# Performance work log

Measured on AMD Instinct MI355X. Metric: run time of the kernel, lower is better.

The kernel has to match this reference:

```python
import jax, jax.numpy as jnp
import numpy as np

N, M, A, F = 8000, 12, 64, 64
EPS = 1e-5


def setup_inputs() -> dict:
    key = jax.random.key(0)
    ks = jax.random.split(key, 8)
    rn = lambda k, s, sc=0.05: jax.random.normal(k, s, jnp.float32) * sc
    return {
        "atom_in_fea": rn(ks[0], (N, A), 1.0),
        "nbr_fea": rn(ks[1], (N, M, F), 1.0),
        "nbr_fea_idx": jax.random.randint(ks[2], (N, M), 0, N),
        # fc_full: in = 2A+F, out = 2A (stored as (in, out))
        "W_full": rn(ks[3], (2 * A + F, 2 * A)), "b_full": jnp.zeros((2 * A,), jnp.float32),
        "bn1_gamma": jnp.ones((2 * A,), jnp.float32), "bn1_beta": jnp.zeros((2 * A,), jnp.float32),
        # fc_edge: in = 2A+F, out = 2F
        "W_edge": rn(ks[4], (2 * A + F, 2 * F)), "b_edge": jnp.zeros((2 * F,), jnp.float32),
        "bne_gamma": jnp.ones((2 * F,), jnp.float32), "bne_beta": jnp.zeros((2 * F,), jnp.float32),
        # fc_3body: in = 3A+2F, out = 2A
        "W_3body": rn(ks[5], (3 * A + 2 * F, 2 * A)), "b_3body": jnp.zeros((2 * A,), jnp.float32),
        "bn3_gamma": jnp.ones((2 * A,), jnp.float32), "bn3_beta": jnp.zeros((2 * A,), jnp.float32),
        # bn2 over atom_fea_len
        "bn2_gamma": jnp.ones((A,), jnp.float32), "bn2_beta": jnp.zeros((A,), jnp.float32),
    }


def _bn(x, gamma, beta):
    # training-mode BatchNorm1d: batch stats over all but the last (channel) axis, biased var
    axes = tuple(range(x.ndim - 1))
    mean = jnp.mean(x, axes, keepdims=True)
    var = jnp.mean(jnp.square(x - mean), axes, keepdims=True)
    return (x - mean) * jax.lax.rsqrt(var + EPS) * gamma + beta


def _gate(z, axis):
    filt, core = jnp.split(z, 2, axis=-1)
    return jnp.sum(jax.nn.sigmoid(filt) * jax.nn.softplus(core), axis=axis)


def reference(atom_in_fea, nbr_fea, nbr_fea_idx,
              W_full, b_full, bn1_gamma, bn1_beta,
              W_edge, b_edge, bne_gamma, bne_beta,
              W_3body, b_3body, bn3_gamma, bn3_beta,
              bn2_gamma, bn2_beta):
    a_len = atom_in_fea.shape[1]
    f_len = nbr_fea.shape[2]
    atom_nbr = atom_in_fea[nbr_fea_idx]                       # (N, M, A) gather
    total = jnp.concatenate([
        jnp.broadcast_to(atom_in_fea[:, None, :], atom_nbr.shape),
        atom_nbr, nbr_fea], axis=-1)                           # (N, M, 2A+F)

    # 2-body gated update
    g = _bn(total @ W_full + b_full, bn1_gamma, bn1_beta)      # (N, M, 2A)
    two_body = _gate(g, axis=1)                                # (N, A)

    # explicit edge update
    e = _bn(total @ W_edge + b_edge, bne_gamma, bne_beta)      # (N, M, 2F)
    ef, ec = jnp.split(e, 2, axis=-1)
    nbr_out_fea = nbr_fea + jax.nn.sigmoid(ef) * jax.nn.softplus(ec)

    # 3-body term: Linear over concat([x_i, x_j, x_l, e_ij, e_il]) decomposed so we never
    # materialize the (N, M, M, 3A+2F) concat; only the (N, M, M, 2A) projection exists.
    Wa, Wj, Wl, Wij, Wil = jnp.split(
        W_3body, [a_len, 2 * a_len, 3 * a_len, 3 * a_len + f_len], axis=0)
    p_i = atom_in_fea @ Wa                                     # (N, 2A)
    p_j = atom_nbr @ Wj + nbr_fea @ Wij                        # (N, M, 2A) j/ij part
    p_l = atom_nbr @ Wl + nbr_fea @ Wil                        # (N, M, 2A) l/il part
    z = p_i[:, None, None, :] + p_j[:, :, None, :] + p_l[:, None, :, :] + b_3body
    z = _bn(z, bn3_gamma, bn3_beta)                            # (N, M, M, 2A)
    three_body = _gate(z, axis=(1, 2))                         # (N, A)

    total_summed = _bn(two_body + three_body, bn2_gamma, bn2_beta)
    atom_out_fea = jax.nn.softplus(atom_in_fea + total_summed)
    return (atom_out_fea, nbr_out_fea)
```

## Files before the change

kernel.cpp:

```cpp
#include <hip/hip_runtime.h>

typedef unsigned short u16;
typedef unsigned int u32;
typedef __attribute__((ext_vector_type(8))) short short8;
typedef __attribute__((ext_vector_type(4))) float f32x4;

#define NATOMS 8000
#define MNBR 12
#define EPSV 1e-5f
#define AB 4
#define ROWS 48
#define NBLK 2000
#define K2REC 1664

#define GRP_B 1056
#define STG_B 12672
__device__ __forceinline__ int stg_idx(int row, int col) {
  return (row >> 2) * 528 + (row & 3) * 128 + col;
}

#define PA_OFF 0
#define WTA_OFF 12288000
#define WTE_OFF 12386304
#define SSUM_OFF 12451840
#define PARAMS_OFF 12459008
#define TBUF_OFF 12462080
#define WS_NEED 14510080

#define SS_BN1S 0
#define SS_BN1S2 128
#define SS_BNES 256
#define SS_BNES2 384
#define SS_U2 512
#define SS_V2 640
#define SS_A 768
#define SS_A2 896
#define SS_UB 1024
#define SS_VB 1152
#define SS_AU 1280
#define SS_AV 1408
#define SS_UV 1536

__device__ __forceinline__ u16 f2bf(float f) {
  u32 u = __float_as_uint(f);
  u += 0x7FFFu + ((u >> 16) & 1u);
  return (u16)(u >> 16);
}
__device__ __forceinline__ float bf2f(u16 h) { return __uint_as_float(((u32)h) << 16); }

__device__ __forceinline__ float sigf(float x) {
  return __builtin_amdgcn_rcpf(1.f + __expf(-x));
}
__device__ __forceinline__ float spf(float x) {
  return fmaxf(x, 0.f) + __logf(1.f + __expf(-fabsf(x)));
}

__device__ __forceinline__ void mfma16(f32x4 &acc, short8 a, short8 b) {
  asm volatile("v_mfma_f32_16x16x32_bf16 %0, %1, %2, %0" : "+v"(acc) : "v"(a), "v"(b));
}
__device__ __forceinline__ void accfence(f32x4 &a) {
  asm volatile("s_nop 7\ns_nop 7\ns_nop 7" : "+v"(a));
}
__device__ __forceinline__ void initfence(f32x4 &a) {
  asm volatile("s_nop 1" : "+v"(a));
}

typedef __attribute__((address_space(3))) unsigned int lds_uint;
typedef __attribute__((address_space(1))) const unsigned int glob_uint;
__device__ __forceinline__ void dma16(const void* g, void* l) {
  __builtin_amdgcn_global_load_lds((glob_uint*)g, (lds_uint*)l, 16, 0, 0);
}

__device__ __forceinline__ void load_idx3(const int* __restrict__ nidx, int eb, int w, int l,
                                          int (&ai)[3]) {
#pragma unroll
  for (int i = 0; i < 3; ++i) ai[i] = nidx[eb + (w * 3 + i) * 4 + (l >> 4)];
}
__device__ __forceinline__ void dma_slice(const u16* __restrict__ PA, const int (&ai)[3],
                                          char* st, int off, int w, int l) {
#pragma unroll
  for (int i = 0; i < 3; ++i) {
    const u16* base = PA + (size_t)ai[i] * 768 + ((l & 15) << 3);
    dma16(base + off, (u16*)st + (w * 3 + i) * 528);
  }
}
__device__ __forceinline__ void dma_own2(const u16* __restrict__ PA, u16* paown0, u16* paown1,
                                         int ab, int l) {
  const u16* src = PA + (size_t)(ab + (l >> 4)) * 768 + ((l & 15) << 3);
  dma16(src, paown0);
  dma16(src + 256, paown1);
}
__device__ __forceinline__ void wait_A_barrier() {
  asm volatile("s_waitcnt vmcnt(3)" ::: "memory");
  __builtin_amdgcn_s_barrier();
}

__device__ __forceinline__ void stage_row16(short* lds, int row, int c16, const float* __restrict__ src) {
  const float4* s4 = reinterpret_cast<const float4*>(src);
  float4 q0 = s4[0], q1 = s4[1], q2 = s4[2], q3 = s4[3];
  short8 lo, hi;
  lo[0]=(short)f2bf(q0.x); lo[1]=(short)f2bf(q0.y); lo[2]=(short)f2bf(q0.z); lo[3]=(short)f2bf(q0.w);
  lo[4]=(short)f2bf(q1.x); lo[5]=(short)f2bf(q1.y); lo[6]=(short)f2bf(q1.z); lo[7]=(short)f2bf(q1.w);
  hi[0]=(short)f2bf(q2.x); hi[1]=(short)f2bf(q2.y); hi[2]=(short)f2bf(q2.z); hi[3]=(short)f2bf(q2.w);
  hi[4]=(short)f2bf(q3.x); hi[5]=(short)f2bf(q3.y); hi[6]=(short)f2bf(q3.z); hi[7]=(short)f2bf(q3.w);
  int base = row * 128 + c16 * 2;
  int sw = (row & 7) << 4;
  *reinterpret_cast<short8*>(reinterpret_cast<char*>(lds) + (base ^ sw)) = lo;
  *reinterpret_cast<short8*>(reinterpret_cast<char*>(lds) + ((base + 16) ^ sw)) = hi;
}

__device__ __forceinline__ short8 lds_afrag(const short* lds, int row, int kbyte) {
  int off = (row * 128 + kbyte) ^ ((row & 7) << 4);
  return *reinterpret_cast<const short8*>(reinterpret_cast<const char*>(lds) + off);
}

template <int RT>
__device__ __forceinline__ void mfma_block(const short* nbrT, const u16* __restrict__ WTE,
                                           int b, int w, int l, f32x4 (&acc)[RT][2]) {
  short8 bfr[2][2];
#pragma unroll
  for (int p = 0; p < 2; ++p) {
    int wr = b * 128 + ((w + p * 4) << 4) + (l & 15);
#pragma unroll
    for (int kc = 0; kc < 2; ++kc)
      bfr[p][kc] = *reinterpret_cast<const short8*>(WTE + (size_t)wr * 64 + kc * 32 + ((l >> 4) << 3));
  }
#pragma unroll
  for (int rt = 0; rt < RT; ++rt)
#pragma unroll
    for (int p = 0; p < 2; ++p) { acc[rt][p] = f32x4{0.f, 0.f, 0.f, 0.f}; initfence(acc[rt][p]); }
#pragma unroll
  for (int rt = 0; rt < RT; ++rt) {
    int arow = rt * 16 + (l & 15);
    short8 a0 = lds_afrag(nbrT, arow, (l >> 4) << 4);
    short8 a1 = lds_afrag(nbrT, arow, 64 + ((l >> 4) << 4));
#pragma unroll
    for (int p = 0; p < 2; ++p) {
      mfma16(acc[rt][p], a0, bfr[p][0]);
      mfma16(acc[rt][p], a1, bfr[p][1]);
    }
  }
#pragma unroll
  for (int rt = 0; rt < RT; ++rt)
#pragma unroll
    for (int p = 0; p < 2; ++p) accfence(acc[rt][p]);
}

__global__ __launch_bounds__(256) void k0_prep(const float* __restrict__ W_full,
                                               const float* __restrict__ W_edge,
                                               const float* __restrict__ W_3body,
                                               u16* __restrict__ WTA, u16* __restrict__ WTE,
                                               float* __restrict__ ssum) {
  int t = blockIdx.x * 256 + threadIdx.x;
  if (t < 1792) ssum[t] = 0.f;
  if (t < 49152) {
    int col = t >> 6, k = t & 63;
    int blk = col >> 7, c = col & 127;
    float v;
    switch (blk) {
      case 0: v = W_full[k * 128 + c]; break;
      case 1: v = W_full[(64 + k) * 128 + c]; break;
      case 2: v = W_edge[k * 128 + c]; break;
      case 3: v = W_edge[(64 + k) * 128 + c]; break;
      case 4: v = W_3body[(64 + k) * 128 + c]; break;
      default: v = W_3body[(128 + k) * 128 + c]; break;
    }
    WTA[t] = f2bf(v);
  } else if (t < 49152 + 32768) {
    int u = t - 49152;
    int col = u >> 6, k = u & 63;
    int blk = col >> 7, c = col & 127;
    float v;
    switch (blk) {
      case 0: v = W_full[(128 + k) * 128 + c]; break;
      case 1: v = W_edge[(128 + k) * 128 + c]; break;
      case 2: v = W_3body[(192 + k) * 128 + c]; break;
      default: v = W_3body[(256 + k) * 128 + c]; break;
    }
    WTE[u] = f2bf(v);
  }
}

__global__ __launch_bounds__(256) void k1_pa(const float* __restrict__ atom_in,
                                             const u16* __restrict__ WTA,
                                             u16* __restrict__ PA) {
  __shared__ __align__(16) short xt[16 * 64];
  int t = threadIdx.x, l = t & 63, w = t >> 6;
  int ab = blockIdx.x * 16;
  if (t < 64) {
    int row = t >> 2, c16 = (t & 3) * 16;
    stage_row16(xt, row, c16, atom_in + (size_t)(ab + row) * 64 + c16);
  }
  __syncthreads();
  short8 a0 = lds_afrag(xt, l & 15, (l >> 4) << 4);
  short8 a1 = lds_afrag(xt, l & 15, 64 + ((l >> 4) << 4));
  for (int q = 0; q < 12; ++q) {
    int colg = (w * 12 + q) * 16 + (l & 15);
    short8 b0 = *reinterpret_cast<const short8*>(WTA + (size_t)colg * 64 + ((l >> 4) << 3));
    short8 b1 = *reinterpret_cast<const short8*>(WTA + (size_t)colg * 64 + 32 + ((l >> 4) << 3));
    f32x4 acc = f32x4{0.f, 0.f, 0.f, 0.f};
    initfence(acc);
    mfma16(acc, a0, b0);
    mfma16(acc, a1, b1);
    accfence(acc);
#pragma unroll
    for (int r = 0; r < 4; ++r) {
      int row = ((l >> 4) << 2) + r;
      PA[(size_t)(ab + row) * 768 + colg] = f2bf(acc[r]);
    }
  }
}

__global__ __launch_bounds__(256, 4) void k2a_stats(const float* __restrict__ nbr_fea,
                                                    const int* __restrict__ nidx,
                                                    const float* __restrict__ b_full,
                                                    const float* __restrict__ b_edge,
                                                    const u16* __restrict__ PA,
                                                    const u16* __restrict__ WTE,
                                                    float* __restrict__ k2scr) {
  __shared__ __align__(16) char smem[33536];
  short* nbrT = (short*)smem;
  u16* paown0 = (u16*)(smem + 31488);
  u16* paown1 = (u16*)(smem + 32512);
  int t = threadIdx.x, l = t & 63, w = t >> 6;
  int ab = blockIdx.x * AB, eb = ab * 12;
  float* sc = k2scr + (size_t)blockIdx.x * K2REC;

  for (int u = t; u < ROWS * 4; u += 256) {
    int row = u >> 2, c16 = (u & 3) * 16;
    stage_row16(nbrT, row, c16, nbr_fea + (size_t)(eb + row) * 64 + c16);
  }
  int ai[3];
  load_idx3(nidx, eb, w, l, ai);
  dma_slice(PA, ai, smem + 6144, 128, w, l);
  if (w == 0) dma_own2(PA, paown0, paown1, ab, l);
  dma_slice(PA, ai, smem + 18816, 384, w, l);
  wait_A_barrier();

#pragma unroll
  for (int b = 0; b < 2; ++b) {
    const u16* stg = (const u16*)(smem + 6144 + b * STG_B);
    const u16* po = b ? paown1 : paown0;
    f32x4 acc[3][2];
    mfma_block<3>(nbrT, WTE, b, w, l, acc);
    int col0 = (w << 4) + (l & 15), col1 = col0 + 64;
    int g = l >> 4;
    const float* bp = b ? b_edge : b_full;
    float bias0 = bp[col0], bias1 = bp[col1];
    float vs0 = 0.f, vs1 = 0.f, q0 = 0.f, q1 = 0.f;
#pragma unroll
    for (int rt = 0; rt < 3; ++rt) {
      int a12 = (rt * 16 + g * 4) / 12;
      float o0 = bf2f(po[a12 * 128 + col0]) + bias0;
      float o1 = bf2f(po[a12 * 128 + col1]) + bias1;
#pragma unroll
      for (int r = 0; r < 4; ++r) {
        int row = rt * 16 + g * 4 + r;
        float v0 = acc[rt][0][r] + bf2f(stg[stg_idx(row, col0)]) + o0;
        float v1 = acc[rt][1][r] + bf2f(stg[stg_idx(row, col1)]) + o1;
        vs0 += v0; q0 += v0 * v0; vs1 += v1; q1 += v1 * v1;
      }
    }
    vs0 += __shfl_xor(vs0, 16); vs0 += __shfl_xor(vs0, 32);
    vs1 += __shfl_xor(vs1, 16); vs1 += __shfl_xor(vs1, 32);
    q0 += __shfl_xor(q0, 16); q0 += __shfl_xor(q0, 32);
    q1 += __shfl_xor(q1, 16); q1 += __shfl_xor(q1, 32);
    if (l < 16) {
      int base = b ? 256 : 0;
      sc[base + col0] = vs0;
      sc[base + 128 + col0] = q0;
      sc[base + col1] = vs1;
      sc[base + 128 + col1] = q1;
    }
    if (b == 0) __syncthreads();
  }
}

__global__ __launch_bounds__(256, 4) void k2b_stats(const float* __restrict__ atom_in,
                                                    const float* __restrict__ nbr_fea,
                                                    const int* __restrict__ nidx,
                                                    const float* __restrict__ W_3body,
                                                    const float* __restrict__ b_3body,
                                                    const u16* __restrict__ PA,
                                                    const u16* __restrict__ WTE,
                                                    float* __restrict__ k2scr) {
  __shared__ __align__(16) char smem[36608];
  short* nbrT   = (short*)smem;
  float* ubar   = (float*)(smem + 31488);
  float* vbar   = (float*)(smem + 33536);
  float* xown   = (float*)(smem + 35584);
  float* redscr = (float*)(smem + 6144);
  int t = threadIdx.x, l = t & 63, w = t >> 6;
  int ab = blockIdx.x * AB, eb = ab * 12;
  float* sc = k2scr + (size_t)blockIdx.x * K2REC;

  for (int u = t; u < ROWS * 4; u += 256) {
    int row = u >> 2, c16 = (u & 3) * 16;
    stage_row16(nbrT, row, c16, nbr_fea + (size_t)(eb + row) * 64 + c16);
  }
  ubar[t] = 0.f; ubar[256 + t] = 0.f; vbar[t] = 0.f; vbar[256 + t] = 0.f;
  xown[t] = atom_in[(size_t)ab * 64 + t];
  int ai[3];
  load_idx3(nidx, eb, w, l, ai);
  dma_slice(PA, ai, smem + 6144, 512, w, l);
  dma_slice(PA, ai, smem + 18816, 640, w, l);
  wait_A_barrier();

#pragma unroll
  for (int b = 2; b < 4; ++b) {
    const u16* stg = (const u16*)(smem + 6144 + (b - 2) * STG_B);
    float* uvb = (b == 2) ? ubar : vbar;
    f32x4 acc[3][2];
    mfma_block<3>(nbrT, WTE, b, w, l, acc);
    int col0 = (w << 4) + (l & 15), col1 = col0 + 64;
    int g = l >> 4;
    float q0 = 0.f, q1 = 0.f;
#pragma unroll
    for (int rt = 0; rt < 3; ++rt) {
      int a12 = (rt * 16 + g * 4) / 12;
      float s0 = 0.f, s1 = 0.f;
#pragma unroll
      for (int r = 0; r < 4; ++r) {
        int row = rt * 16 + g * 4 + r;
        float v0 = acc[rt][0][r] + bf2f(stg[stg_idx(row, col0)]);
        float v1 = acc[rt][1][r] + bf2f(stg[stg_idx(row, col1)]);
        s0 += v0; q0 += v0 * v0; s1 += v1; q1 += v1 * v1;
      }
      atomicAdd(&uvb[a12 * 128 + col0], s0);
      atomicAdd(&uvb[a12 * 128 + col1], s1);
    }
    q0 += __shfl_xor(q0, 16); q0 += __shfl_xor(q0, 32);
    q1 += __shfl_xor(q1, 16); q1 += __shfl_xor(q1, 32);
    if (l < 16) {
      int base = (b == 2) ? SS_U2 : SS_V2;
      sc[base + col0] = q0;
      sc[base + col1] = q1;
    }
    if (b == 2) __syncthreads();
  }
  __syncthreads();

  {
    int c = t & 127, h = t >> 7;
    float dv0 = 0.f, dv1 = 0.f;
#pragma unroll 4
    for (int k = 0; k < 64; ++k) {
      float wk = W_3body[k * 128 + c];
      dv0 += xown[(2 * h) * 64 + k] * wk;
      dv1 += xown[(2 * h + 1) * 64 + k] * wk;
    }
    float b3v = b_3body[c];
    float pA = 0.f, pA2 = 0.f, pUb = 0.f, pVb = 0.f, pAU = 0.f, pAV = 0.f, pUV = 0.f;
#pragma unroll
    for (int aa = 0; aa < 2; ++aa) {
      int a = 2 * h + aa;
      float aval = (aa ? dv1 : dv0) + b3v;
      float ub = ubar[a * 128 + c] * (1.f / 12.f);
      float vb = vbar[a * 128 + c] * (1.f / 12.f);
      pA += aval; pA2 += aval * aval; pUb += ub; pVb += vb;
      pAU += aval * ub; pAV += aval * vb; pUV += ub * vb;
    }
    if (h == 1) {
      float* rs = &redscr[c * 7];
      rs[0] = pA; rs[1] = pA2; rs[2] = pUb; rs[3] = pVb; rs[4] = pAU; rs[5] = pAV; rs[6] = pUV;
    }
    __syncthreads();
    if (h == 0) {
      const float* rs = &redscr[c * 7];
      sc[SS_A + c] = pA + rs[0];
      sc[SS_A2 + c] = pA2 + rs[1];
      sc[SS_UB + c] = pUb + rs[2];
      sc[SS_VB + c] = pVb + rs[3];
      sc[SS_AU + c] = pAU + rs[4];
      sc[SS_AV + c] = pAV + rs[5];
      sc[SS_UV + c] = pUV + rs[6];
    }
  }
}

__global__ __launch_bounds__(256) void k3r_reduce(const float* __restrict__ k2scr,
                                                  float* __restrict__ ssum) {
  int cb = blockIdx.x & 1, ch = blockIdx.x >> 1;
  int f = cb * 256 + threadIdx.x;
  if (f >= K2REC / 4) return;
  int r0 = ch * 32;
  if (r0 >= NBLK) return;
  int r1 = min(r0 + 32, NBLK);
  float s0 = 0.f, s1 = 0.f, s2 = 0.f, s3 = 0.f;
#pragma unroll 8
  for (int r = r0; r < r1; ++r) {
    float4 v = *reinterpret_cast<const float4*>(k2scr + (size_t)r * K2REC + f * 4);
    s0 += v.x; s1 += v.y; s2 += v.z; s3 += v.w;
  }
  atomicAdd(&ssum[f * 4 + 0], s0);
  atomicAdd(&ssum[f * 4 + 1], s1);
  atomicAdd(&ssum[f * 4 + 2], s2);
  atomicAdd(&ssum[f * 4 + 3], s3);
}

__global__ void k3p_params(const float* __restrict__ ssum,
                           const float* __restrict__ g1, const float* __restrict__ be1,
                           const float* __restrict__ ge, const float* __restrict__ bee,
                           const float* __restrict__ g3, const float* __restrict__ be3,
                           float* __restrict__ params) {
  int c = threadIdx.x;
  if (c >= 128) return;
  const float cnt1 = 1.f / 96000.f;
  {
    float m = ssum[SS_BN1S + c] * cnt1;
    float var = ssum[SS_BN1S2 + c] * cnt1 - m * m;
    float s = g1[c] * rsqrtf(fmaxf(var, 0.f) + EPSV);
    params[c] = s; params[128 + c] = be1[c] - m * s;
  }
  {
    float m = ssum[SS_BNES + c] * cnt1;
    float var = ssum[SS_BNES2 + c] * cnt1 - m * m;
    float s = ge[c] * rsqrtf(fmaxf(var, 0.f) + EPSV);
    params[256 + c] = s; params[384 + c] = bee[c] - m * s;
  }
  {
    float Nf = (float)NATOMS;
    float A_ = ssum[SS_A + c], A2 = ssum[SS_A2 + c];
    float U2 = ssum[SS_U2 + c], V2 = ssum[SS_V2 + c];
    float Ub = ssum[SS_UB + c], Vb = ssum[SS_VB + c];
    float AU = ssum[SS_AU + c], AV = ssum[SS_AV + c], UV = ssum[SS_UV + c];
    float m = (A_ + Ub + Vb) / Nf;
    float ez2 = A2 / Nf + (U2 + V2) / (Nf * 12.f) + 2.f * (AU + AV + UV) / Nf;
    float var = ez2 - m * m;
    float s = g3[c] * rsqrtf(fmaxf(var, 0.f) + EPSV);
    params[512 + c] = s; params[640 + c] = be3[c] - m * s;
  }
}

__global__ __launch_bounds__(256, 4) void k4a_main(const float* __restrict__ nbr_fea,
                                                   const int* __restrict__ nidx,
                                                   const float* __restrict__ b_full,
                                                   const float* __restrict__ b_edge,
                                                   const u16* __restrict__ PA,
                                                   const u16* __restrict__ WTE,
                                                   const float* __restrict__ params,
                                                   float* __restrict__ tbuf,
                                                   float* __restrict__ out_nbr) {
  __shared__ __align__(16) char smem[36608];
  short* nbrT     = (short*)smem;
  u16* paown0     = (u16*)(smem + 31488);
  u16* paown1     = (u16*)(smem + 32512);
  float* t2buf    = (float*)(smem + 33536);
  float* params_s = (float*)(smem + 34560);
  int t = threadIdx.x, l = t & 63, w = t >> 6;
  int ab = blockIdx.x * AB, eb = ab * 12;

  for (int u = t; u < ROWS * 4; u += 256) {
    int row = u >> 2, c16 = (u & 3) * 16;
    stage_row16(nbrT, row, c16, nbr_fea + (size_t)(eb + row) * 64 + c16);
  }
  params_s[t] = params[t];
  params_s[t + 256] = params[t + 256];
  t2buf[t] = 0.f;
  int ai[3];
  load_idx3(nidx, eb, w, l, ai);
  dma_slice(PA, ai, smem + 6144, 128, w, l);
  if (w == 0) dma_own2(PA, paown0, paown1, ab, l);
  dma_slice(PA, ai, smem + 18816, 384, w, l);
  wait_A_barrier();

#pragma unroll
  for (int b = 0; b < 2; ++b) {
    const u16* stg = (const u16*)(smem + 6144 + b * STG_B);
    const u16* po = b ? paown1 : paown0;
    f32x4 acc[3][2];
    mfma_block<3>(nbrT, WTE, b, w, l, acc);
    int col0 = (w << 4) + (l & 15), col1 = col0 + 64;
    int g = l >> 4;
    const float* bp = b ? b_edge : b_full;
    float bias0 = bp[col0], bias1 = bp[col1];
    float sc0 = params_s[b * 256 + col0], sh0 = params_s[b * 256 + 128 + col0];
    float sc1 = params_s[b * 256 + col1], sh1 = params_s[b * 256 + 128 + col1];
#pragma unroll
    for (int rt = 0; rt < 3; ++rt) {
      int a12 = (rt * 16 + g * 4) / 12;
      float o0 = bf2f(po[a12 * 128 + col0]) + bias0;
      float o1 = bf2f(po[a12 * 128 + col1]) + bias1;
      float gsum = 0.f;
#pragma unroll
      for (int r = 0; r < 4; ++r) {
        int row = rt * 16 + g * 4 + r;
        float v0 = acc[rt][0][r] + bf2f(stg[stg_idx(row, col0)]) + o0;
        float v1 = acc[rt][1][r] + bf2f(stg[stg_idx(row, col1)]) + o1;
        float gate = sigf(v0 * sc0 + sh0) * spf(v1 * sc1 + sh1);
        if (b == 0) {
          gsum += gate;
        } else {
          size_t eg = (size_t)(eb + row) * 64 + col0;
          out_nbr[eg] = nbr_fea[eg] + gate;
        }
      }
      if (b == 0) atomicAdd(&t2buf[a12 * 64 + col0], gsum);
    }
    __syncthreads();
  }
  tbuf[(size_t)(ab + w) * 64 + l] = t2buf[t];
}

__global__ __launch_bounds__(256, 4) void k4b_main(const float* __restrict__ atom_in,
                                                   const float* __restrict__ nbr_fea,
                                                   const int* __restrict__ nidx,
                                                   const float* __restrict__ W_3body,
                                                   const float* __restrict__ b_3body,
                                                   const u16* __restrict__ PA,
                                                   const u16* __restrict__ WTE,
                                                   const float* __restrict__ params,
                                                   float* __restrict__ tbuf,
                                                   float* __restrict__ bn2scr) {
  __shared__ __align__(16) char smem[35584];
  short* nbrT    = (short*)smem;
  u16* stage2    = (u16*)(smem + 6144);
  u16* stage3    = (u16*)(smem + 18816);
  float* a_s     = (float*)(smem + 31488);
  float* xown    = (float*)(smem + 33536);
  float* p3_s    = (float*)(smem + 34560);
  float* redscr2 = (float*)(smem + 6144);
  int t = threadIdx.x, l = t & 63, w = t >> 6;
  int ab = blockIdx.x * AB, eb = ab * 12;

  for (int u = t; u < ROWS * 4; u += 256) {
    int row = u >> 2, c16 = (u & 3) * 16;
    stage_row16(nbrT, row, c16, nbr_fea + (size_t)(eb + row) * 64 + c16);
  }
  xown[t] = atom_in[(size_t)ab * 64 + t];
  p3_s[t] = params[512 + t];
  float two_body = tbuf[(size_t)(ab + w) * 64 + l];
  int ai[3];
  load_idx3(nidx, eb, w, l, ai);
  dma_slice(PA, ai, smem + 6144, 512, w, l);
  dma_slice(PA, ai, smem + 18816, 640, w, l);
  wait_A_barrier();

  {
    int c = t & 127, h = t >> 7;
    float dv0 = 0.f, dv1 = 0.f;
#pragma unroll 4
    for (int k = 0; k < 64; ++k) {
      float wk = W_3body[k * 128 + c];
      dv0 += xown[(2 * h) * 64 + k] * wk;
      dv1 += xown[(2 * h + 1) * 64 + k] * wk;
    }
    float s3 = p3_s[c], t3 = p3_s[128 + c];
    float b3v = b_3body[c];
    a_s[(2 * h) * 128 + c] = (dv0 + b3v) * s3 + t3;
    a_s[(2 * h + 1) * 128 + c] = (dv1 + b3v) * s3 + t3;
  }

#pragma unroll
  for (int b = 2; b < 4; ++b) {
    u16* stg = (b == 2) ? stage2 : stage3;
    f32x4 acc[3][2];
    mfma_block<3>(nbrT, WTE, b, w, l, acc);
    int col0 = (w << 4) + (l & 15), col1 = col0 + 64;
    int g = l >> 4;
    float s30 = p3_s[col0], s31 = p3_s[col1];
#pragma unroll
    for (int rt = 0; rt < 3; ++rt) {
#pragma unroll
      for (int r = 0; r < 4; ++r) {
        int row = rt * 16 + g * 4 + r;
        float v0 = (acc[rt][0][r] + bf2f(stg[stg_idx(row, col0)])) * s30;
        float v1 = (acc[rt][1][r] + bf2f(stg[stg_idx(row, col1)])) * s31;
        stg[stg_idx(row, col0)] = f2bf(v0);
        stg[stg_idx(row, col1)] = f2bf(v1);
      }
    }
    if (b == 2) __syncthreads();
  }
  __syncthreads();

  float acc3 = 0.f;
  {
    int c = l, a = w;
    float af = a_s[a * 128 + c], ac = a_s[a * 128 + 64 + c];
    float Fl[12], Hl[12];
#pragma unroll
    for (int j2 = 0; j2 < 12; ++j2) {
      float vf = bf2f(stage3[stg_idx(a * 12 + j2, c)]);
      float vc = bf2f(stage3[stg_idx(a * 12 + j2, 64 + c)]);
      Fl[j2] = __expf(-vf);
      Hl[j2] = __expf(vc);
    }
    for (int j = 0; j < 12; ++j) {
      float uf = bf2f(stage2[stg_idx(a * 12 + j, c)]);
      float uc = bf2f(stage2[stg_idx(a * 12 + j, 64 + c)]);
      float Ej = __expf(-(af + uf));
      float Gj = __expf(ac + uc);
#pragma unroll
      for (int l2 = 0; l2 < 12; ++l2) {
        float p = fmaf(Ej, Fl[l2], 1.f);
        float q = fmaf(Gj, Hl[l2], 1.f);
        acc3 += __builtin_amdgcn_rcpf(p) * __log2f(q);
      }
    }
  }
  __syncthreads();

  {
    float x = two_body + acc3 * 0.6931471805599453f;
    tbuf[(size_t)(ab + w) * 64 + l] = x;
    redscr2[t] = x;
    redscr2[256 + t] = x * x;
    __syncthreads();
    if (t < 64) {
      float s = redscr2[t] + redscr2[t + 64] + redscr2[t + 128] + redscr2[t + 192];
      float s2 = redscr2[256 + t] + redscr2[256 + t + 64] + redscr2[256 + t + 128] + redscr2[256 + t + 192];
      bn2scr[(size_t)t * 2048 + blockIdx.x] = s;
      bn2scr[(size_t)(64 + t) * 2048 + blockIdx.x] = s2;
    }
  }
}

__global__ __launch_bounds__(256) void k5_reduce(const float* __restrict__ bn2scr,
                                                 float* __restrict__ bn2sum) {
  __shared__ float wsum[4];
  int c = blockIdx.x, t = threadIdx.x;
  float s = 0.f;
#pragma unroll 4
  for (int i = t; i < NBLK; i += 256) s += bn2scr[(size_t)c * 2048 + i];
  s += __shfl_xor(s, 1); s += __shfl_xor(s, 2); s += __shfl_xor(s, 4);
  s += __shfl_xor(s, 8); s += __shfl_xor(s, 16); s += __shfl_xor(s, 32);
  if ((t & 63) == 0) wsum[t >> 6] = s;
  __syncthreads();
  if (t == 0) bn2sum[c] = wsum[0] + wsum[1] + wsum[2] + wsum[3];
}

__global__ __launch_bounds__(256) void k6_out(const float* __restrict__ atom_in,
                                              const float* __restrict__ tbuf,
                                              const float* __restrict__ bn2sum,
                                              const float* __restrict__ g2,
                                              const float* __restrict__ be2,
                                              float* __restrict__ out_atom) {
  __shared__ float sc[64], sh[64];
  int t = threadIdx.x;
  if (t < 64) {
    float S = bn2sum[t], S2 = bn2sum[64 + t];
    float m = S * (1.f / (float)NATOMS);
    float var = S2 * (1.f / (float)NATOMS) - m * m;
    float s = g2[t] * rsqrtf(fmaxf(var, 0.f) + EPSV);
    sc[t] = s; sh[t] = be2[t] - m * s;
  }
  __syncthreads();
  int i = blockIdx.x * 256 + t;
  if (i < NATOMS * 64) {
    int c = i & 63;
    float v = atom_in[i] + tbuf[i] * sc[c] + sh[c];
    out_atom[i] = spf(v);
  }
}

extern "C" void kernel_launch(void* const* d_in, const int* in_sizes, int n_in,
                              void* d_out, int out_size, void* d_ws, size_t ws_size,
                              hipStream_t stream) {
  if (ws_size < (size_t)WS_NEED) return;
  const float* atom_in = (const float*)d_in[0];
  const float* nbr_fea = (const float*)d_in[1];
  const int* nidx = (const int*)d_in[2];
  const float* W_full = (const float*)d_in[3];
  const float* b_full = (const float*)d_in[4];
  const float* g1 = (const float*)d_in[5];
  const float* be1 = (const float*)d_in[6];
  const float* W_edge = (const float*)d_in[7];
  const float* b_edge = (const float*)d_in[8];
  const float* ge = (const float*)d_in[9];
  const float* bee = (const float*)d_in[10];
  const float* W_3body = (const float*)d_in[11];
  const float* b_3body = (const float*)d_in[12];
  const float* g3 = (const float*)d_in[13];
  const float* be3 = (const float*)d_in[14];
  const float* g2 = (const float*)d_in[15];
  const float* be2 = (const float*)d_in[16];

  char* ws = (char*)d_ws;
  u16* PA = (u16*)(ws + PA_OFF);
  u16* WTA = (u16*)(ws + WTA_OFF);
  u16* WTE = (u16*)(ws + WTE_OFF);
  float* ssum = (float*)(ws + SSUM_OFF);
  float* bn2sum = ssum + K2REC;
  float* params = (float*)(ws + PARAMS_OFF);
  float* tbuf = (float*)(ws + TBUF_OFF);

  float* out_atom = (float*)d_out;
  float* out_nbr = out_atom + NATOMS * 64;
  float* k2scr = out_nbr;
  float* bn2scr = out_atom;

  k0_prep<<<320, 256, 0, stream>>>(W_full, W_edge, W_3body, WTA, WTE, ssum);
  k1_pa<<<500, 256, 0, stream>>>(atom_in, WTA, PA);
  k2a_stats<<<NBLK, 256, 0, stream>>>(nbr_fea, nidx, b_full, b_edge, PA, WTE, k2scr);
  k2b_stats<<<NBLK, 256, 0, stream>>>(atom_in, nbr_fea, nidx, W_3body, b_3body, PA, WTE, k2scr);
  k3r_reduce<<<128, 256, 0, stream>>>(k2scr, ssum);
  k3p_params<<<1, 128, 0, stream>>>(ssum, g1, be1, ge, bee, g3, be3, params);
  k4a_main<<<NBLK, 256, 0, stream>>>(nbr_fea, nidx, b_full, b_edge, PA, WTE, params, tbuf, out_nbr);
  k4b_main<<<NBLK, 256, 0, stream>>>(atom_in, nbr_fea, nidx, W_3body, b_3body, PA, WTE, params,
                                     tbuf, bn2scr);
  k5_reduce<<<128, 256, 0, stream>>>(bn2scr, bn2sum);
  k6_out<<<2000, 256, 0, stream>>>(atom_in, tbuf, bn2sum, g2, be2, out_atom);
}
```

Before: 177.8 us.

## Replace precomputed atom projections with on-the-fly gathered bf16 atom features

Drops the k1_pa kernel, which precomputed a 768-wide bf16 projection per atom (PA, ~12MB). Each main/stats kernel now gathers 64-wide bf16 atom rows (XB) for neighbours and recomputes the projections with extra MFMAs (mfma_dual/mfma_own) alongside the edge matmul. The goal is to cut gather traffic and LDS footprint, since rows are 128B instead of large PA slices, at the cost of doubling MFMA work per block. It also adds a transposed fp32 Wa copy for vectorised dot products and removes some barriers.

```diff
diff --git a/kernel.cpp b/kernel.cpp
--- a/kernel.cpp
+++ b/kernel.cpp
@@ -13,19 +13,19 @@
 #define NBLK 2000
 #define K2REC 1664
 
-#define GRP_B 1056
 #define STG_B 12672
 __device__ __forceinline__ int stg_idx(int row, int col) {
   return (row >> 2) * 528 + (row & 3) * 128 + col;
 }
 
-#define PA_OFF 0
-#define WTA_OFF 12288000
-#define WTE_OFF 12386304
-#define SSUM_OFF 12451840
-#define PARAMS_OFF 12459008
-#define TBUF_OFF 12462080
-#define WS_NEED 14510080
+#define XB_OFF 0
+#define WTA_OFF 1024000
+#define WTE_OFF 1122304
+#define WAT_OFF 1187840
+#define SSUM_OFF 1220608
+#define PARAMS_OFF 1227776
+#define TBUF_OFF 1230848
+#define WS_NEED 3278848
 
 #define SS_BN1S 0
 #define SS_BN1S2 128
@@ -65,36 +65,6 @@
   asm volatile("s_nop 1" : "+v"(a));
 }
 
-typedef __attribute__((address_space(3))) unsigned int lds_uint;
-typedef __attribute__((address_space(1))) const unsigned int glob_uint;
-__device__ __forceinline__ void dma16(const void* g, void* l) {
-  __builtin_amdgcn_global_load_lds((glob_uint*)g, (lds_uint*)l, 16, 0, 0);
-}
-
-__device__ __forceinline__ void load_idx3(const int* __restrict__ nidx, int eb, int w, int l,
-                                          int (&ai)[3]) {
-#pragma unroll
-  for (int i = 0; i < 3; ++i) ai[i] = nidx[eb + (w * 3 + i) * 4 + (l >> 4)];
-}
-__device__ __forceinline__ void dma_slice(const u16* __restrict__ PA, const int (&ai)[3],
-                                          char* st, int off, int w, int l) {
-#pragma unroll
-  for (int i = 0; i < 3; ++i) {
-    const u16* base = PA + (size_t)ai[i] * 768 + ((l & 15) << 3);
-    dma16(base + off, (u16*)st + (w * 3 + i) * 528);
-  }
-}
-__device__ __forceinline__ void dma_own2(const u16* __restrict__ PA, u16* paown0, u16* paown1,
-                                         int ab, int l) {
-  const u16* src = PA + (size_t)(ab + (l >> 4)) * 768 + ((l & 15) << 3);
-  dma16(src, paown0);
-  dma16(src + 256, paown1);
-}
-__device__ __forceinline__ void wait_A_barrier() {
-  asm volatile("s_waitcnt vmcnt(3)" ::: "memory");
-  __builtin_amdgcn_s_barrier();
-}
-
 __device__ __forceinline__ void stage_row16(short* lds, int row, int c16, const float* __restrict__ src) {
   const float4* s4 = reinterpret_cast<const float4*>(src);
   float4 q0 = s4[0], q1 = s4[1], q2 = s4[2], q3 = s4[3];
@@ -109,21 +79,41 @@
   *reinterpret_cast<short8*>(reinterpret_cast<char*>(lds) + ((base + 16) ^ sw)) = hi;
 }
 
+__device__ __forceinline__ void stage_xj(const u16* __restrict__ XB, const int* __restrict__ nidx,
+                                         int eb, int ab, char* xjT, int t) {
+  for (int s = t; s < 512; s += 256) {
+    int r = s >> 3, j = s & 7;
+    uint4 val = make_uint4(0u, 0u, 0u, 0u);
+    if (r < 48) {
+      int idx = nidx[eb + r];
+      val = *reinterpret_cast<const uint4*>(XB + (size_t)idx * 64 + j * 8);
+    } else if (r < 52) {
+      val = *reinterpret_cast<const uint4*>(XB + (size_t)(ab + r - 48) * 64 + j * 8);
+    }
+    int off = (r * 128 + j * 16) ^ ((r & 7) << 4);
+    *reinterpret_cast<uint4*>(xjT + off) = val;
+  }
+}
+
 __device__ __forceinline__ short8 lds_afrag(const short* lds, int row, int kbyte) {
   int off = (row * 128 + kbyte) ^ ((row & 7) << 4);
   return *reinterpret_cast<const short8*>(reinterpret_cast<const char*>(lds) + off);
 }
 
 template <int RT>
-__device__ __forceinline__ void mfma_block(const short* nbrT, const u16* __restrict__ WTE,
-                                           int b, int w, int l, f32x4 (&acc)[RT][2]) {
-  short8 bfr[2][2];
+__device__ __forceinline__ void mfma_dual(const short* xjT, const short* nbrT,
+                                          const u16* __restrict__ WTA, const u16* __restrict__ WTE,
+                                          int baseA, int baseE, int w, int l,
+                                          f32x4 (&acc)[RT][2]) {
+  short8 ba[2][2], be[2][2];
 #pragma unroll
   for (int p = 0; p < 2; ++p) {
-    int wr = b * 128 + ((w + p * 4) << 4) + (l & 15);
-#pragma unroll
-    for (int kc = 0; kc < 2; ++kc)
-      bfr[p][kc] = *reinterpret_cast<const short8*>(WTE + (size_t)wr * 64 + kc * 32 + ((l >> 4) << 3));
+    int colg = ((w + p * 4) << 4) + (l & 15);
+#pragma unroll
+    for (int kc = 0; kc < 2; ++kc) {
+      ba[p][kc] = *reinterpret_cast<const short8*>(WTA + (size_t)(baseA + colg) * 64 + kc * 32 + ((l >> 4) << 3));
+      be[p][kc] = *reinterpret_cast<const short8*>(WTE + (size_t)(baseE + colg) * 64 + kc * 32 + ((l >> 4) << 3));
+    }
   }
 #pragma unroll
   for (int rt = 0; rt < RT; ++rt)
@@ -132,12 +122,16 @@
 #pragma unroll
   for (int rt = 0; rt < RT; ++rt) {
     int arow = rt * 16 + (l & 15);
-    short8 a0 = lds_afrag(nbrT, arow, (l >> 4) << 4);
-    short8 a1 = lds_afrag(nbrT, arow, 64 + ((l >> 4) << 4));
+    short8 x0 = lds_afrag(xjT, arow, (l >> 4) << 4);
+    short8 x1 = lds_afrag(xjT, arow, 64 + ((l >> 4) << 4));
+    short8 n0 = lds_afrag(nbrT, arow, (l >> 4) << 4);
+    short8 n1 = lds_afrag(nbrT, arow, 64 + ((l >> 4) << 4));
 #pragma unroll
     for (int p = 0; p < 2; ++p) {
-      mfma16(acc[rt][p], a0, bfr[p][0]);
-      mfma16(acc[rt][p], a1, bfr[p][1]);
+      mfma16(acc[rt][p], x0, ba[p][0]);
+      mfma16(acc[rt][p], x1, ba[p][1]);
+      mfma16(acc[rt][p], n0, be[p][0]);
+      mfma16(acc[rt][p], n1, be[p][1]);
     }
   }
 #pragma unroll
@@ -146,13 +140,64 @@
     for (int p = 0; p < 2; ++p) accfence(acc[rt][p]);
 }
 
-__global__ __launch_bounds__(256) void k0_prep(const float* __restrict__ W_full,
+__device__ __forceinline__ void mfma_own(const short* xjT, const u16* __restrict__ WTA,
+                                         int baseO, int w, int l, float* ownv) {
+  short8 bo[2][2];
+#pragma unroll
+  for (int p = 0; p < 2; ++p) {
+    int colg = ((w + p * 4) << 4) + (l & 15);
+#pragma unroll
+    for (int kc = 0; kc < 2; ++kc)
+      bo[p][kc] = *reinterpret_cast<const short8*>(WTA + (size_t)(baseO + colg) * 64 + kc * 32 + ((l >> 4) << 3));
+  }
+  int arow = 48 + (l & 15);
+  short8 x0 = lds_afrag(xjT, arow, (l >> 4) << 4);
+  short8 x1 = lds_afrag(xjT, arow, 64 + ((l >> 4) << 4));
+  f32x4 acc[2];
+#pragma unroll
+  for (int p = 0; p < 2; ++p) {
+    acc[p] = f32x4{0.f, 0.f, 0.f, 0.f};
+    initfence(acc[p]);
+    mfma16(acc[p], x0, bo[p][0]);
+    mfma16(acc[p], x1, bo[p][1]);
+  }
+#pragma unroll
+  for (int p = 0; p < 2; ++p) accfence(acc[p]);
+  if (l < 16) {
+    int col0 = (w << 4) + l;
+#pragma unroll
+    for (int r = 0; r < 4; ++r) {
+      ownv[r * 128 + col0] = acc[0][r];
+      ownv[r * 128 + col0 + 64] = acc[1][r];
+    }
+  }
+}
+
+__device__ __forceinline__ void aterm_dot(const float* __restrict__ WaT, const float* xown,
+                                          int c, int h, float& dv0, float& dv1) {
+  const float4* wa4 = reinterpret_cast<const float4*>(WaT + (size_t)c * 64);
+  const float4* x0 = reinterpret_cast<const float4*>(xown + (2 * h) * 64);
+  const float4* x1 = reinterpret_cast<const float4*>(xown + (2 * h + 1) * 64);
+  dv0 = 0.f; dv1 = 0.f;
+#pragma unroll
+  for (int q = 0; q < 16; ++q) {
+    float4 wv = wa4[q], a4 = x0[q], b4 = x1[q];
+    dv0 += a4.x * wv.x + a4.y * wv.y + a4.z * wv.z + a4.w * wv.w;
+    dv1 += b4.x * wv.x + b4.y * wv.y + b4.z * wv.z + b4.w * wv.w;
+  }
+}
+
+__global__ __launch_bounds__(256) void k0_prep(const float* __restrict__ atom_in,
+                                               const float* __restrict__ W_full,
                                                const float* __restrict__ W_edge,
                                                const float* __restrict__ W_3body,
+                                               u16* __restrict__ XB,
                                                u16* __restrict__ WTA, u16* __restrict__ WTE,
+                                               float* __restrict__ WaT,
                                                float* __restrict__ ssum) {
   int t = blockIdx.x * 256 + threadIdx.x;
   if (t < 1792) ssum[t] = 0.f;
+  if (t < 8192) { int c = t >> 6, k = t & 63; WaT[t] = W_3body[k * 128 + c]; }
   if (t < 49152) {
     int col = t >> 6, k = t & 63;
     int blk = col >> 7, c = col & 127;
@@ -166,7 +211,7 @@
       default: v = W_3body[(128 + k) * 128 + c]; break;
     }
     WTA[t] = f2bf(v);
-  } else if (t < 49152 + 32768) {
+  } else if (t < 81920) {
     int u = t - 49152;
     int col = u >> 6, k = u & 63;
     int blk = col >> 7, c = col & 127;
@@ -179,49 +224,21 @@
     }
     WTE[u] = f2bf(v);
   }
-}
-
-__global__ __launch_bounds__(256) void k1_pa(const float* __restrict__ atom_in,
-                                             const u16* __restrict__ WTA,
-                                             u16* __restrict__ PA) {
-  __shared__ __align__(16) short xt[16 * 64];
-  int t = threadIdx.x, l = t & 63, w = t >> 6;
-  int ab = blockIdx.x * 16;
-  if (t < 64) {
-    int row = t >> 2, c16 = (t & 3) * 16;
-    stage_row16(xt, row, c16, atom_in + (size_t)(ab + row) * 64 + c16);
-  }
-  __syncthreads();
-  short8 a0 = lds_afrag(xt, l & 15, (l >> 4) << 4);
-  short8 a1 = lds_afrag(xt, l & 15, 64 + ((l >> 4) << 4));
-  for (int q = 0; q < 12; ++q) {
-    int colg = (w * 12 + q) * 16 + (l & 15);
-    short8 b0 = *reinterpret_cast<const short8*>(WTA + (size_t)colg * 64 + ((l >> 4) << 3));
-    short8 b1 = *reinterpret_cast<const short8*>(WTA + (size_t)colg * 64 + 32 + ((l >> 4) << 3));
-    f32x4 acc = f32x4{0.f, 0.f, 0.f, 0.f};
-    initfence(acc);
-    mfma16(acc, a0, b0);
-    mfma16(acc, a1, b1);
-    accfence(acc);
-#pragma unroll
-    for (int r = 0; r < 4; ++r) {
-      int row = ((l >> 4) << 2) + r;
-      PA[(size_t)(ab + row) * 768 + colg] = f2bf(acc[r]);
-    }
-  }
+  if (t < NATOMS * 64) XB[t] = f2bf(atom_in[t]);
 }
 
 __global__ __launch_bounds__(256, 4) void k2a_stats(const float* __restrict__ nbr_fea,
                                                     const int* __restrict__ nidx,
                                                     const float* __restrict__ b_full,
                                                     const float* __restrict__ b_edge,
-                                                    const u16* __restrict__ PA,
+                                                    const u16* __restrict__ XB,
+                                                    const u16* __restrict__ WTA,
                                                     const u16* __restrict__ WTE,
                                                     float* __restrict__ k2scr) {
-  __shared__ __align__(16) char smem[33536];
+  __shared__ __align__(16) char smem[16384];
   short* nbrT = (short*)smem;
-  u16* paown0 = (u16*)(smem + 31488);
-  u16* paown1 = (u16*)(smem + 32512);
+  char* xjT   = smem + 6144;
+  float* ownv = (float*)(smem + 14336);
   int t = threadIdx.x, l = t & 63, w = t >> 6;
   int ab = blockIdx.x * AB, eb = ab * 12;
   float* sc = k2scr + (size_t)blockIdx.x * K2REC;
@@ -230,19 +247,14 @@
     int row = u >> 2, c16 = (u & 3) * 16;
     stage_row16(nbrT, row, c16, nbr_fea + (size_t)(eb + row) * 64 + c16);
   }
-  int ai[3];
-  load_idx3(nidx, eb, w, l, ai);
-  dma_slice(PA, ai, smem + 6144, 128, w, l);
-  if (w == 0) dma_own2(PA, paown0, paown1, ab, l);
-  dma_slice(PA, ai, smem + 18816, 384, w, l);
-  wait_A_barrier();
+  stage_xj(XB, nidx, eb, ab, xjT, t);
+  __syncthreads();
 
 #pragma unroll
   for (int b = 0; b < 2; ++b) {
-    const u16* stg = (const u16*)(smem + 6144 + b * STG_B);
-    const u16* po = b ? paown1 : paown0;
     f32x4 acc[3][2];
-    mfma_block<3>(nbrT, WTE, b, w, l, acc);
+    mfma_dual<3>((short*)xjT, nbrT, WTA, WTE, b ? 384 : 128, b * 128, w, l, acc);
+    mfma_own((short*)xjT, WTA, b ? 256 : 0, w, l, ownv);
     int col0 = (w << 4) + (l & 15), col1 = col0 + 64;
     int g = l >> 4;
     const float* bp = b ? b_edge : b_full;
@@ -251,13 +263,12 @@
 #pragma unroll
     for (int rt = 0; rt < 3; ++rt) {
       int a12 = (rt * 16 + g * 4) / 12;
-      float o0 = bf2f(po[a12 * 128 + col0]) + bias0;
-      float o1 = bf2f(po[a12 * 128 + col1]) + bias1;
+      float o0 = ownv[a12 * 128 + col0] + bias0;
+      float o1 = ownv[a12 * 128 + col1] + bias1;
 #pragma unroll
       for (int r = 0; r < 4; ++r) {
-        int row = rt * 16 + g * 4 + r;
-        float v0 = acc[rt][0][r] + bf2f(stg[stg_idx(row, col0)]) + o0;
-        float v1 = acc[rt][1][r] + bf2f(stg[stg_idx(row, col1)]) + o1;
+        float v0 = acc[rt][0][r] + o0;
+        float v1 = acc[rt][1][r] + o1;
         vs0 += v0; q0 += v0 * v0; vs1 += v1; q1 += v1 * v1;
       }
     }
@@ -272,24 +283,25 @@
       sc[base + col1] = vs1;
       sc[base + 128 + col1] = q1;
     }
-    if (b == 0) __syncthreads();
   }
 }
 
 __global__ __launch_bounds__(256, 4) void k2b_stats(const float* __restrict__ atom_in,
                                                     const float* __restrict__ nbr_fea,
                                                     const int* __restrict__ nidx,
-                                                    const float* __restrict__ W_3body,
+                                                    const float* __restrict__ WaT,
                                                     const float* __restrict__ b_3body,
-                                                    const u16* __restrict__ PA,
+                                                    const u16* __restrict__ XB,
+                                                    const u16* __restrict__ WTA,
                                                     const u16* __restrict__ WTE,
                                                     float* __restrict__ k2scr) {
-  __shared__ __align__(16) char smem[36608];
+  __shared__ __align__(16) char smem[23040];
   short* nbrT   = (short*)smem;
-  float* ubar   = (float*)(smem + 31488);
-  float* vbar   = (float*)(smem + 33536);
-  float* xown   = (float*)(smem + 35584);
-  float* redscr = (float*)(smem + 6144);
+  char* xjT     = smem + 6144;
+  float* ubar   = (float*)(smem + 14336);
+  float* vbar   = (float*)(smem + 16384);
+  float* xown   = (float*)(smem + 18432);
+  float* redscr = (float*)(smem + 19456);
   int t = threadIdx.x, l = t & 63, w = t >> 6;
   int ab = blockIdx.x * AB, eb = ab * 12;
   float* sc = k2scr + (size_t)blockIdx.x * K2REC;
@@ -298,20 +310,16 @@
     int row = u >> 2, c16 = (u & 3) * 16;
     stage_row16(nbrT, row, c16, nbr_fea + (size_t)(eb + row) * 64 + c16);
   }
+  stage_xj(XB, nidx, eb, ab, xjT, t);
   ubar[t] = 0.f; ubar[256 + t] = 0.f; vbar[t] = 0.f; vbar[256 + t] = 0.f;
   xown[t] = atom_in[(size_t)ab * 64 + t];
-  int ai[3];
-  load_idx3(nidx, eb, w, l, ai);
-  dma_slice(PA, ai, smem + 6144, 512, w, l);
-  dma_slice(PA, ai, smem + 18816, 640, w, l);
-  wait_A_barrier();
+  __syncthreads();
 
 #pragma unroll
   for (int b = 2; b < 4; ++b) {
-    const u16* stg = (const u16*)(smem + 6144 + (b - 2) * STG_B);
+    f32x4 acc[3][2];
+    mfma_dual<3>((short*)xjT, nbrT, WTA, WTE, (b == 2) ? 512 : 640, b * 128, w, l, acc);
     float* uvb = (b == 2) ? ubar : vbar;
-    f32x4 acc[3][2];
-    mfma_block<3>(nbrT, WTE, b, w, l, acc);
     int col0 = (w << 4) + (l & 15), col1 = col0 + 64;
     int g = l >> 4;
     float q0 = 0.f, q1 = 0.f;
@@ -321,9 +329,8 @@
       float s0 = 0.f, s1 = 0.f;
 #pragma unroll
       for (int r = 0; r < 4; ++r) {
-        int row = rt * 16 + g * 4 + r;
-        float v0 = acc[rt][0][r] + bf2f(stg[stg_idx(row, col0)]);
-        float v1 = acc[rt][1][r] + bf2f(stg[stg_idx(row, col1)]);
+        float v0 = acc[rt][0][r];
+        float v1 = acc[rt][1][r];
         s0 += v0; q0 += v0 * v0; s1 += v1; q1 += v1 * v1;
       }
       atomicAdd(&uvb[a12 * 128 + col0], s0);
@@ -336,19 +343,13 @@
       sc[base + col0] = q0;
       sc[base + col1] = q1;
     }
-    if (b == 2) __syncthreads();
   }
   __syncthreads();
 
   {
     int c = t & 127, h = t >> 7;
-    float dv0 = 0.f, dv1 = 0.f;
-#pragma unroll 4
-    for (int k = 0; k < 64; ++k) {
-      float wk = W_3body[k * 128 + c];
-      dv0 += xown[(2 * h) * 64 + k] * wk;
-      dv1 += xown[(2 * h + 1) * 64 + k] * wk;
-    }
+    float dv0, dv1;
+    aterm_dot(WaT, xown, c, h, dv0, dv1);
     float b3v = b_3body[c];
     float pA = 0.f, pA2 = 0.f, pUb = 0.f, pVb = 0.f, pAU = 0.f, pAV = 0.f, pUV = 0.f;
 #pragma unroll
@@ -436,17 +437,18 @@
                                                    const int* __restrict__ nidx,
                                                    const float* __restrict__ b_full,
                                                    const float* __restrict__ b_edge,
-                                                   const u16* __restrict__ PA,
+                                                   const u16* __restrict__ XB,
+                                                   const u16* __restrict__ WTA,
                                                    const u16* __restrict__ WTE,
                                                    const float* __restrict__ params,
                                                    float* __restrict__ tbuf,
                                                    float* __restrict__ out_nbr) {
-  __shared__ __align__(16) char smem[36608];
+  __shared__ __align__(16) char smem[19456];
   short* nbrT     = (short*)smem;
-  u16* paown0     = (u16*)(smem + 31488);
-  u16* paown1     = (u16*)(smem + 32512);
-  float* t2buf    = (float*)(smem + 33536);
-  float* params_s = (float*)(smem + 34560);
+  char* xjT       = smem + 6144;
+  float* ownv     = (float*)(smem + 14336);
+  float* t2buf    = (float*)(smem + 16384);
+  float* params_s = (float*)(smem + 17408);
   int t = threadIdx.x, l = t & 63, w = t >> 6;
   int ab = blockIdx.x * AB, eb = ab * 12;
 
@@ -454,22 +456,17 @@
     int row = u >> 2, c16 = (u & 3) * 16;
     stage_row16(nbrT, row, c16, nbr_fea + (size_t)(eb + row) * 64 + c16);
   }
+  stage_xj(XB, nidx, eb, ab, xjT, t);
   params_s[t] = params[t];
   params_s[t + 256] = params[t + 256];
   t2buf[t] = 0.f;
-  int ai[3];
-  load_idx3(nidx, eb, w, l, ai);
-  dma_slice(PA, ai, smem + 6144, 128, w, l);
-  if (w == 0) dma_own2(PA, paown0, paown1, ab, l);
-  dma_slice(PA, ai, smem + 18816, 384, w, l);
-  wait_A_barrier();
+  __syncthreads();
 
 #pragma unroll
   for (int b = 0; b < 2; ++b) {
-    const u16* stg = (const u16*)(smem + 6144 + b * STG_B);
-    const u16* po = b ? paown1 : paown0;
     f32x4 acc[3][2];
-    mfma_block<3>(nbrT, WTE, b, w, l, acc);
+    mfma_dual<3>((short*)xjT, nbrT, WTA, WTE, b ? 384 : 128, b * 128, w, l, acc);
+    mfma_own((short*)xjT, WTA, b ? 256 : 0, w, l, ownv);
     int col0 = (w << 4) + (l & 15), col1 = col0 + 64;
     int g = l >> 4;
     const float* bp = b ? b_edge : b_full;
@@ -479,14 +476,14 @@
 #pragma unroll
     for (int rt = 0; rt < 3; ++rt) {
       int a12 = (rt * 16 + g * 4) / 12;
-      float o0 = bf2f(po[a12 * 128 + col0]) + bias0;
-      float o1 = bf2f(po[a12 * 128 + col1]) + bias1;
+      float o0 = ownv[a12 * 128 + col0] + bias0;
+      float o1 = ownv[a12 * 128 + col1] + bias1;
       float gsum = 0.f;
 #pragma unroll
       for (int r = 0; r < 4; ++r) {
         int row = rt * 16 + g * 4 + r;
-        float v0 = acc[rt][0][r] + bf2f(stg[stg_idx(row, col0)]) + o0;
-        float v1 = acc[rt][1][r] + bf2f(stg[stg_idx(row, col1)]) + o1;
+        float v0 = acc[rt][0][r] + o0;
+        float v1 = acc[rt][1][r] + o1;
         float gate = sigf(v0 * sc0 + sh0) * spf(v1 * sc1 + sh1);
         if (b == 0) {
           gsum += gate;
@@ -497,29 +494,31 @@
       }
       if (b == 0) atomicAdd(&t2buf[a12 * 64 + col0], gsum);
     }
-    __syncthreads();
-  }
+  }
+  __syncthreads();
   tbuf[(size_t)(ab + w) * 64 + l] = t2buf[t];
 }
 
 __global__ __launch_bounds__(256, 4) void k4b_main(const float* __restrict__ atom_in,
                                                    const float* __restrict__ nbr_fea,
                                                    const int* __restrict__ nidx,
-                                                   const float* __restrict__ W_3body,
+                                                   const float* __restrict__ WaT,
                                                    const float* __restrict__ b_3body,
-                                                   const u16* __restrict__ PA,
+                                                   const u16* __restrict__ XB,
+                                                   const u16* __restrict__ WTA,
                                                    const u16* __restrict__ WTE,
                                                    const float* __restrict__ params,
                                                    float* __restrict__ tbuf,
                                                    float* __restrict__ bn2scr) {
-  __shared__ __align__(16) char smem[35584];
+  __shared__ __align__(16) char smem[31104];
   short* nbrT    = (short*)smem;
-  u16* stage2    = (u16*)(smem + 6144);
-  u16* stage3    = (u16*)(smem + 18816);
-  float* a_s     = (float*)(smem + 31488);
-  float* xown    = (float*)(smem + 33536);
-  float* p3_s    = (float*)(smem + 34560);
-  float* redscr2 = (float*)(smem + 6144);
+  char* xjT      = smem + 6144;
+  u16* u_s       = (u16*)(smem + 14336);
+  float* a_s     = (float*)(smem + 27008);
+  float* xown    = (float*)(smem + 29056);
+  float* p3_s    = (float*)(smem + 30080);
+  u16* v_s       = (u16*)smem;
+  float* redscr2 = (float*)(smem + 14336);
   int t = threadIdx.x, l = t & 63, w = t >> 6;
   int ab = blockIdx.x * AB, eb = ab * 12;
 
@@ -527,35 +526,25 @@
     int row = u >> 2, c16 = (u & 3) * 16;
     stage_row16(nbrT, row, c16, nbr_fea + (size_t)(eb + row) * 64 + c16);
   }
+  stage_xj(XB, nidx, eb, ab, xjT, t);
   xown[t] = atom_in[(size_t)ab * 64 + t];
   p3_s[t] = params[512 + t];
   float two_body = tbuf[(size_t)(ab + w) * 64 + l];
-  int ai[3];
-  load_idx3(nidx, eb, w, l, ai);
-  dma_slice(PA, ai, smem + 6144, 512, w, l);
-  dma_slice(PA, ai, smem + 18816, 640, w, l);
-  wait_A_barrier();
+  __syncthreads();
 
   {
     int c = t & 127, h = t >> 7;
-    float dv0 = 0.f, dv1 = 0.f;
-#pragma unroll 4
-    for (int k = 0; k < 64; ++k) {
-      float wk = W_3body[k * 128 + c];
-      dv0 += xown[(2 * h) * 64 + k] * wk;
-      dv1 += xown[(2 * h + 1) * 64 + k] * wk;
-    }
+    float dv0, dv1;
+    aterm_dot(WaT, xown, c, h, dv0, dv1);
     float s3 = p3_s[c], t3 = p3_s[128 + c];
     float b3v = b_3body[c];
     a_s[(2 * h) * 128 + c] = (dv0 + b3v) * s3 + t3;
     a_s[(2 * h + 1) * 128 + c] = (dv1 + b3v) * s3 + t3;
   }
 
-#pragma unroll
-  for (int b = 2; b < 4; ++b) {
-    u16* stg = (b == 2) ? stage2 : stage3;
+  {
     f32x4 acc[3][2];
-    mfma_block<3>(nbrT, WTE, b, w, l, acc);
+    mfma_dual<3>((short*)xjT, nbrT, WTA, WTE, 512, 256, w, l, acc);
     int col0 = (w << 4) + (l & 15), col1 = col0 + 64;
     int g = l >> 4;
     float s30 = p3_s[col0], s31 = p3_s[col1];
@@ -564,13 +553,27 @@
 #pragma unroll
       for (int r = 0; r < 4; ++r) {
         int row = rt * 16 + g * 4 + r;
-        float v0 = (acc[rt][0][r] + bf2f(stg[stg_idx(row, col0)])) * s30;
-        float v1 = (acc[rt][1][r] + bf2f(stg[stg_idx(row, col1)])) * s31;
-        stg[stg_idx(row, col0)] = f2bf(v0);
-        stg[stg_idx(row, col1)] = f2bf(v1);
+        u_s[stg_idx(row, col0)] = f2bf(acc[rt][0][r] * s30);
+        u_s[stg_idx(row, col1)] = f2bf(acc[rt][1][r] * s31);
       }
     }
-    if (b == 2) __syncthreads();
+  }
+  {
+    f32x4 acc[3][2];
+    mfma_dual<3>((short*)xjT, nbrT, WTA, WTE, 640, 384, w, l, acc);
+    __syncthreads();
+    int col0 = (w << 4) + (l & 15), col1 = col0 + 64;
+    int g = l >> 4;
+    float s30 = p3_s[col0], s31 = p3_s[col1];
+#pragma unroll
+    for (int rt = 0; rt < 3; ++rt) {
+#pragma unroll
+      for (int r = 0; r < 4; ++r) {
+        int row = rt * 16 + g * 4 + r;
+        v_s[stg_idx(row, col0)] = f2bf(acc[rt][0][r] * s30);
+        v_s[stg_idx(row, col1)] = f2bf(acc[rt][1][r] * s31);
+      }
+    }
   }
   __syncthreads();
 
@@ -581,14 +584,14 @@
     float Fl[12], Hl[12];
 #pragma unroll
     for (int j2 = 0; j2 < 12; ++j2) {
-      float vf = bf2f(stage3[stg_idx(a * 12 + j2, c)]);
-      float vc = bf2f(stage3[stg_idx(a * 12 + j2, 64 + c)]);
+      float vf = bf2f(v_s[stg_idx(a * 12 + j2, c)]);
+      float vc = bf2f(v_s[stg_idx(a * 12 + j2, 64 + c)]);
       Fl[j2] = __expf(-vf);
       Hl[j2] = __expf(vc);
     }
     for (int j = 0; j < 12; ++j) {
-      float uf = bf2f(stage2[stg_idx(a * 12 + j, c)]);
-      float uc = bf2f(stage2[stg_idx(a * 12 + j, 64 + c)]);
+      float uf = bf2f(u_s[stg_idx(a * 12 + j, c)]);
+      float uc = bf2f(u_s[stg_idx(a * 12 + j, 64 + c)]);
       float Ej = __expf(-(af + uf));
       float Gj = __expf(ac + uc);
 #pragma unroll
@@ -677,9 +680,10 @@
   const float* be2 = (const float*)d_in[16];
 
   char* ws = (char*)d_ws;
-  u16* PA = (u16*)(ws + PA_OFF);
+  u16* XB = (u16*)(ws + XB_OFF);
   u16* WTA = (u16*)(ws + WTA_OFF);
   u16* WTE = (u16*)(ws + WTE_OFF);
+  float* WaT = (float*)(ws + WAT_OFF);
   float* ssum = (float*)(ws + SSUM_OFF);
   float* bn2sum = ssum + K2REC;
   float* params = (float*)(ws + PARAMS_OFF);
@@ -690,14 +694,13 @@
   float* k2scr = out_nbr;
   float* bn2scr = out_atom;
 
-  k0_prep<<<320, 256, 0, stream>>>(W_full, W_edge, W_3body, WTA, WTE, ssum);
-  k1_pa<<<500, 256, 0, stream>>>(atom_in, WTA, PA);
-  k2a_stats<<<NBLK, 256, 0, stream>>>(nbr_fea, nidx, b_full, b_edge, PA, WTE, k2scr);
-  k2b_stats<<<NBLK, 256, 0, stream>>>(atom_in, nbr_fea, nidx, W_3body, b_3body, PA, WTE, k2scr);
+  k0_prep<<<2000, 256, 0, stream>>>(atom_in, W_full, W_edge, W_3body, XB, WTA, WTE, WaT, ssum);
+  k2a_stats<<<NBLK, 256, 0, stream>>>(nbr_fea, nidx, b_full, b_edge, XB, WTA, WTE, k2scr);
+  k2b_stats<<<NBLK, 256, 0, stream>>>(atom_in, nbr_fea, nidx, WaT, b_3body, XB, WTA, WTE, k2scr);
   k3r_reduce<<<128, 256, 0, stream>>>(k2scr, ssum);
   k3p_params<<<1, 128, 0, stream>>>(ssum, g1, be1, ge, bee, g3, be3, params);
-  k4a_main<<<NBLK, 256, 0, stream>>>(nbr_fea, nidx, b_full, b_edge, PA, WTE, params, tbuf, out_nbr);
-  k4b_main<<<NBLK, 256, 0, stream>>>(atom_in, nbr_fea, nidx, W_3body, b_3body, PA, WTE, params,
+  k4a_main<<<NBLK, 256, 0, stream>>>(nbr_fea, nidx, b_full, b_edge, XB, WTA, WTE, params, tbuf, out_nbr);
+  k4b_main<<<NBLK, 256, 0, stream>>>(atom_in, nbr_fea, nidx, WaT, b_3body, XB, WTA, WTE, params,
                                      tbuf, bn2scr);
   k5_reduce<<<128, 256, 0, stream>>>(bn2scr, bn2sum);
   k6_out<<<2000, 256, 0, stream>>>(atom_in, tbuf, bn2sum, g2, be2, out_atom);
```

Measured after the change: 183.2 us. 1.03x slower.
